# Kernel optimization log

Hardware: AMD Instinct MI355X
Metric: run time of the kernel (lower is better)

## Reference

```python
import jax, jax.numpy as jnp
import numpy as np

B, T, D, H, E, S, K = 2, 2048, 768, 1536, 8, 1, 2
STD = 0.02


def setup_inputs() -> dict:
    key = jax.random.key(0)
    ks = jax.random.split(key, 8)
    x = jax.random.normal(ks[0], (B, T, D), jnp.float32)
    router_w = jax.random.normal(ks[1], (E, D), jnp.float32) * STD
    sw1 = jax.random.normal(ks[2], (S, D, H), jnp.float32) * STD
    sw2 = jax.random.normal(ks[3], (S, D, H), jnp.float32) * STD
    sproj = jax.random.normal(ks[4], (S, H, D), jnp.float32) * STD
    ew1 = jax.random.normal(ks[5], (E, D, H), jnp.float32) * STD
    ew2 = jax.random.normal(ks[6], (E, D, H), jnp.float32) * STD
    eproj = jax.random.normal(ks[7], (E, H, D), jnp.float32) * STD
    return {"x": x, "router_w": router_w, "sw1": sw1, "sw2": sw2,
            "sproj": sproj, "ew1": ew1, "ew2": ew2, "eproj": eproj,
            "top_k": K}


def reference(x, router_w, sw1, sw2, sproj, ew1, ew2, eproj, top_k):
    n_experts = router_w.shape[0]
    # Shared experts (SwiGLU), summed over the shared-expert axis s.
    a = jnp.einsum('btd,sdh->bsth', x, sw1)
    b = jnp.einsum('btd,sdh->bsth', x, sw2)
    shared_out = jnp.einsum('bsth,shd->btd', jax.nn.silu(a) * b, sproj)  # [B,T,D]

    # Router: note the original applies softmax and calls the result `logits`,
    # returning it as the second output.
    probs = jax.nn.softmax(jnp.einsum('btd,ed->bte', x, router_w), axis=-1)  # [B,T,E]
    top_vals, top_idx = jax.lax.top_k(probs, top_k)
    weights = top_vals / jnp.sum(top_vals, axis=-1, keepdims=True)  # renormalized [B,T,K]

    # Dense combine weights: combine[b,t,e] = sum_k weights[b,t,k] * 1[top_idx[b,t,k]==e]
    combine = jnp.sum(jax.nn.one_hot(top_idx, n_experts, dtype=x.dtype)
                      * weights[..., None], axis=-2)  # [B,T,E]

    # Routed experts: compute every expert densely, then mask/weight by combine.
    ea = jnp.einsum('btd,edh->bteh', x, ew1)
    eb = jnp.einsum('btd,edh->bteh', x, ew2)
    routed = jnp.einsum('bteh,ehd,bte->btd', jax.nn.silu(ea) * eb, eproj, combine)

    return shared_out + routed, probs
```

## Files before the change

### kernel.cpp

```cpp
#include <hip/hip_runtime.h>

typedef unsigned short u16;
typedef __bf16 bf16x8 __attribute__((ext_vector_type(8)));
typedef float f32x4 __attribute__((ext_vector_type(4)));

__device__ __forceinline__ u16 f2bf(float f) {
  union { float f; unsigned u; } v; v.f = f;
  return (u16)((v.u + 0x7fffu + ((v.u >> 16) & 1u)) >> 16);
}

#define GLDS16(g, l)                                                          \
  __builtin_amdgcn_global_load_lds(                                           \
      (const __attribute__((address_space(1))) void*)(g),                     \
      (__attribute__((address_space(3))) void*)(l), 16, 0, 0)

#define SBAR()  __builtin_amdgcn_s_barrier()
#define SCHED() __builtin_amdgcn_sched_barrier(0)
#define VMCNT(n) asm volatile("s_waitcnt vmcnt(" #n ")" ::: "memory")

#define NTOK 4096
#define DIM  768
#define HID  1536
#define NEXP 8
#define CAPR 9216
#define SHB  9216
#define NSLOT 13312
#define MAXT 104


__global__ __launch_bounds__(256) void k_tr_all(const float* __restrict__ ew1,
                                                const float* __restrict__ sw1,
                                                const float* __restrict__ ew2,
                                                const float* __restrict__ sw2,
                                                const float* __restrict__ eproj,
                                                const float* __restrict__ sproj,
                                                u16* __restrict__ dstBase) {
  __shared__ u16 tile[64][65];
  constexpr size_t SL = (size_t)HID * DIM;
  const int z = blockIdx.z;
  const float* src;
  int R, C, bxx = blockIdx.x, byy = blockIdx.y;
  if (z < 9)       { src = (z < 8) ? ew1 + (size_t)z * SL : sw1; R = DIM; C = HID; }
  else if (z < 18) { const int q = z - 9;  src = (q < 8) ? ew2 + (size_t)q * SL : sw2; R = DIM; C = HID; }
  else             { const int q = z - 18; src = (q < 8) ? eproj + (size_t)q * SL : sproj;
                     R = HID; C = DIM; const int t = bxx; bxx = byy; byy = t; }
  u16* dst = dstBase + (size_t)z * SL;
  const int c0 = bxx * 64, r0 = byy * 64;
  const int tx = threadIdx.x, ty = threadIdx.y;
  #pragma unroll
  for (int i = 0; i < 16; i++)
    tile[ty + 4 * i][tx] = f2bf(src[(size_t)(r0 + ty + 4 * i) * C + c0 + tx]);
  __syncthreads();
  #pragma unroll
  for (int i = 0; i < 16; i++)
    dst[(size_t)(c0 + ty + 4 * i) * R + r0 + tx] = tile[tx][ty + 4 * i];
}

__global__ __launch_bounds__(64) void k_router(const float* __restrict__ x,
                                               const float* __restrict__ rw,
                                               float* __restrict__ probs,
                                               int* __restrict__ topIdx,
                                               float* __restrict__ topW,
                                               u16* __restrict__ xb) {
  const int t = blockIdx.x;
  const int lane = threadIdx.x;
  const float* xr = x + (size_t)t * DIM;
  u16* xbr = xb + (size_t)t * DIM;
  float acc[NEXP] = {0, 0, 0, 0, 0, 0, 0, 0};
  #pragma unroll
  for (int i = 0; i < DIM / 64; i++) {
    const int d = lane + 64 * i;
    const float xv = xr[d];
    xbr[d] = f2bf(xv);
    #pragma unroll
    for (int e = 0; e < NEXP; e++) acc[e] += xv * rw[e * DIM + d];
  }
  #pragma unroll
  for (int e = 0; e < NEXP; e++)
    #pragma unroll
    for (int s = 32; s > 0; s >>= 1) acc[e] += __shfl_xor(acc[e], s, 64);
  if (lane == 0) {
    float mx = acc[0];
    #pragma unroll
    for (int e = 1; e < NEXP; e++) mx = fmaxf(mx, acc[e]);
    float p[NEXP], sum = 0.f;
    #pragma unroll
    for (int e = 0; e < NEXP; e++) { p[e] = expf(acc[e] - mx); sum += p[e]; }
    const float inv = 1.f / sum;
    #pragma unroll
    for (int e = 0; e < NEXP; e++) p[e] *= inv;
    #pragma unroll
    for (int e = 0; e < NEXP; e++) probs[(size_t)t * NEXP + e] = p[e];
    int i1 = 0;
    #pragma unroll
    for (int e = 1; e < NEXP; e++) if (p[e] > p[i1]) i1 = e;
    int i2 = (i1 == 0) ? 1 : 0;
    #pragma unroll
    for (int e = 0; e < NEXP; e++) if (e != i1 && p[e] > p[i2]) i2 = e;
    const float s2 = 1.f / (p[i1] + p[i2]);
    topIdx[2 * t] = i1; topIdx[2 * t + 1] = i2;
    topW[2 * t] = p[i1] * s2; topW[2 * t + 1] = p[i2] * s2;
  }
}

__global__ __launch_bounds__(256) void k_build(const int* __restrict__ topIdx,
                                               const float* __restrict__ topW,
                                               int* __restrict__ listT,
                                               float* __restrict__ listW,
                                               int* __restrict__ listP,
                                               int* __restrict__ cnt) {
  const int e = blockIdx.x;
  const int tid = threadIdx.x, w = tid >> 6, lane = tid & 63;
  __shared__ int wt[4];
  int base = 0;
  for (int c = 0; c < NTOK / 256; ++c) {
    const int t = c * 256 + tid;
    const int i0 = topIdx[2 * t], i1 = topIdx[2 * t + 1];
    const int pr = (i0 == e) ? 1 : ((i1 == e) ? 2 : 0);
    const unsigned long long m = __ballot(pr != 0);
    const int wl = __popcll(m & ((1ull << lane) - 1ull));
    if (lane == 0) wt[w] = __popcll(m);
    __syncthreads();
    int wbase = 0;
    #pragma unroll
    for (int j = 0; j < 4; j++) if (j < w) wbase += wt[j];
    if (pr) {
      const int pos = base + wbase + wl;
      listT[e * NTOK + pos] = t;
      listW[e * NTOK + pos] = (pr == 1) ? topW[2 * t] : topW[2 * t + 1];
      listP[e * NTOK + pos] = pr;
    }
    base += wt[0] + wt[1] + wt[2] + wt[3];
    __syncthreads();
  }
  if (tid == 0) cnt[e] = base;
}

__global__ __launch_bounds__(256) void k_tilemap(const int* __restrict__ cnt,
                                                 const int* __restrict__ listT,
                                                 const float* __restrict__ listW,
                                                 const int* __restrict__ listP,
                                                 int* __restrict__ tileExp,
                                                 int* __restrict__ tileM0,
                                                 int* __restrict__ slotTok,
                                                 float* __restrict__ slotW,
                                                 int* __restrict__ tokSlot) {
  __shared__ int offPad[NEXP + 1];
  __shared__ int cs[NEXP];
  const int tid = threadIdx.x;
  if (tid == 0) {
    int tt = 0, acc = 0;
    for (int e = 0; e < NEXP; e++) {
      cs[e] = cnt[e];
      offPad[e] = acc;
      const int tiles = (cs[e] + 127) >> 7;
      for (int i = 0; i < tiles; i++) { tileExp[tt] = e; tileM0[tt] = acc + i * 128; tt++; }
      acc += tiles * 128;
    }
    offPad[NEXP] = acc;
    for (int i = 0; i < NTOK / 128; i++) { tileExp[tt] = NEXP; tileM0[tt] = SHB + i * 128; tt++; }
    for (; tt < MAXT; tt++) tileExp[tt] = -1;
  }
  __syncthreads();
  for (int s = tid; s < CAPR; s += 256) {
    int tok = 0; float wv = 0.f; int pp = 0;
    #pragma unroll
    for (int e = 0; e < NEXP; e++)
      if (s >= offPad[e] && s < offPad[e + 1]) {
        const int i = s - offPad[e];
        if (i < cs[e]) {
          tok = listT[e * NTOK + i];
          wv = listW[e * NTOK + i];
          pp = listP[e * NTOK + i];
        }
      }
    slotTok[s] = tok; slotW[s] = wv;
    if (pp) tokSlot[2 * tok + (pp - 1)] = s;
  }
  for (int s = tid; s < NTOK; s += 256) { slotTok[SHB + s] = s; slotW[SHB + s] = 1.f; }
}

__global__ __launch_bounds__(256, 2) void k_gemm1(const u16* __restrict__ xb,
                                                  const u16* __restrict__ w1t,
                                                  const u16* __restrict__ w2t,
                                                  const int* __restrict__ tileExp,
                                                  const int* __restrict__ tileM0,
                                                  const int* __restrict__ slotTok,
                                                  const float* __restrict__ slotW,
                                                  u16* __restrict__ hidden) {
  __shared__ alignas(16) u16 As[3][4096];
  __shared__ alignas(16) u16 B1s[3][4096];
  __shared__ alignas(16) u16 B2s[3][4096];
  const int chunk = (MAXT * (HID / 128)) >> 3;
  const int bid = blockIdx.x;
  const int wgid = (bid & 7) * chunk + (bid >> 3);
  const int bx = wgid % MAXT;
  const int by = wgid / MAXT;
  const int e = tileExp[bx];
  if (e < 0) return;
  const int m0 = tileM0[bx];
  const int nBase = by * 128;
  constexpr size_t SL = (size_t)HID * DIM;
  const u16* w1 = w1t + (size_t)e * SL;
  const u16* w2 = w2t + (size_t)e * SL;
  const int tid = threadIdx.x, w = tid >> 6, lane = tid & 63;
  const int wr = w >> 1, wc = w & 1;

  const int qrow = lane >> 2;
  const int col0 = ((lane & 3) ^ ((lane >> 3) & 3)) * 8;
  const int tok0 = slotTok[m0 + w * 32 + qrow];
  const int tok1 = slotTok[m0 + w * 32 + 16 + qrow];
  const u16* gA0 = xb + (size_t)tok0 * DIM + col0;
  const u16* gA1 = xb + (size_t)tok1 * DIM + col0;
  const u16* gB1a = w1 + (size_t)(nBase + w * 32 + qrow) * DIM + col0;
  const u16* gB1b = w1 + (size_t)(nBase + w * 32 + 16 + qrow) * DIM + col0;
  const u16* gB2a = w2 + (size_t)(nBase + w * 32 + qrow) * DIM + col0;
  const u16* gB2b = w2 + (size_t)(nBase + w * 32 + 16 + qrow) * DIM + col0;
  const int l0 = (w * 2 + 0) * 512 + lane * 8;
  const int l1 = (w * 2 + 1) * 512 + lane * 8;

  f32x4 acc1[4][4], acc2[4][4];
  const f32x4 vz = {0.f, 0.f, 0.f, 0.f};
  #pragma unroll
  for (int m = 0; m < 4; m++)
    #pragma unroll
    for (int n = 0; n < 4; n++) { acc1[m][n] = vz; acc2[m][n] = vz; }

  const int rbase = lane & 15;
  const int swz = (lane >> 4) ^ ((rbase >> 1) & 3);
  const int aoffB = (wr * 64 + rbase) * 32 + swz * 8;
  const int boffB = (wc * 64 + rbase) * 32 + swz * 8;

#define G1_STAGE(buf, kk) do {                                                \
    GLDS16(gA0  + (kk), &As[buf][l0]);  GLDS16(gA1  + (kk), &As[buf][l1]);    \
    GLDS16(gB1a + (kk), &B1s[buf][l0]); GLDS16(gB1b + (kk), &B1s[buf][l1]);   \
    GLDS16(gB2a + (kk), &B2s[buf][l0]); GLDS16(gB2b + (kk), &B2s[buf][l1]);   \
  } while (0)

#define G1_BODY(buf, vm, dostage, kk) do {                                    \
    SCHED(); VMCNT(vm); SBAR(); SCHED();                                      \
    if (dostage) { G1_STAGE((buf + 2) % 3, kk); SCHED(); }                    \
    bf16x8 av[4], b1v[4], b2v[4];                                             \
    _Pragma("unroll")                                                         \
    for (int m = 0; m < 4; m++) av[m] = *(const bf16x8*)&As[buf][aoffB + m * 512]; \
    _Pragma("unroll")                                                         \
    for (int n = 0; n < 4; n++) {                                             \
      b1v[n] = *(const bf16x8*)&B1s[buf][boffB + n * 512];                    \
      b2v[n] = *(const bf16x8*)&B2s[buf][boffB + n * 512];                    \
    }                                                                         \
    __builtin_amdgcn_s_setprio(1);                                            \
    _Pragma("unroll")                                                         \
    for (int m = 0; m < 4; m++)                                               \
      _Pragma("unroll")                                                       \
      for (int n = 0; n < 4; n++) {                                           \
        acc1[m][n] = __builtin_amdgcn_mfma_f32_16x16x32_bf16(av[m], b1v[n], acc1[m][n], 0, 0, 0); \
        acc2[m][n] = __builtin_amdgcn_mfma_f32_16x16x32_bf16(av[m], b2v[n], acc2[m][n], 0, 0, 0); \
      }                                                                       \
    __builtin_amdgcn_s_setprio(0);                                            \
  } while (0)

  G1_STAGE(0, 0);  SCHED();
  G1_STAGE(1, 32); SCHED();
  for (int t = 0; t < 21; t += 3) {
    G1_BODY(0, 6, true, (t + 2) * 32);
    G1_BODY(1, 6, true, (t + 3) * 32);
    G1_BODY(2, 6, true, (t + 4) * 32);
  }
  G1_BODY(0, 6, true, 23 * 32);
  G1_BODY(1, 6, false, 0);
  G1_BODY(2, 0, false, 0);
#undef G1_BODY
#undef G1_STAGE

  #pragma unroll
  for (int m = 0; m < 4; m++)
    #pragma unroll
    for (int r = 0; r < 4; r++) {
      const int slot = m0 + wr * 64 + m * 16 + (lane >> 4) * 4 + r;
      const float cwv = slotW[slot];
      #pragma unroll
      for (int n = 0; n < 4; n++) {
        const int hcol = nBase + wc * 64 + n * 16 + (lane & 15);
        const float v1 = acc1[m][n][r], v2 = acc2[m][n][r];
        hidden[(size_t)slot * HID + hcol] = f2bf((v1 / (1.f + __expf(-v1))) * v2 * cwv);
      }
    }
}

__global__ __launch_bounds__(256, 3) void k_gemm2(const u16* __restrict__ hid,
                                                  const u16* __restrict__ pjt,
                                                  const int* __restrict__ tileExp,
                                                  const int* __restrict__ tileM0,
                                                  float* __restrict__ g2) {
  __shared__ alignas(16) u16 As[3][4096];
  __shared__ alignas(16) u16 Bs[3][4096];
  const int chunk = (MAXT * (DIM / 128)) >> 3;
  const int bid = blockIdx.x;
  const int wgid = (bid & 7) * chunk + (bid >> 3);
  const int bx = wgid % MAXT;
  const int by = wgid / MAXT;
  const int e = tileExp[bx];
  if (e < 0) return;
  const int m0 = tileM0[bx];
  const int nBase = by * 128;
  constexpr size_t SL = (size_t)HID * DIM;
  const u16* pj = pjt + (size_t)e * SL;
  const int tid = threadIdx.x, w = tid >> 6, lane = tid & 63;
  const int wr = w >> 1, wc = w & 1;

  const int qrow = lane >> 2;
  const int col0 = ((lane & 3) ^ ((lane >> 3) & 3)) * 8;
  const u16* gA0 = hid + (size_t)(m0 + w * 32 + qrow) * HID + col0;
  const u16* gA1 = hid + (size_t)(m0 + w * 32 + 16 + qrow) * HID + col0;
  const u16* gBa = pj + (size_t)(nBase + w * 32 + qrow) * HID + col0;
  const u16* gBb = pj + (size_t)(nBase + w * 32 + 16 + qrow) * HID + col0;
  const int l0 = (w * 2 + 0) * 512 + lane * 8;
  const int l1 = (w * 2 + 1) * 512 + lane * 8;

  f32x4 acc[4][4];
  const f32x4 vz = {0.f, 0.f, 0.f, 0.f};
  #pragma unroll
  for (int m = 0; m < 4; m++)
    #pragma unroll
    for (int n = 0; n < 4; n++) acc[m][n] = vz;

  const int rbase = lane & 15;
  const int swz = (lane >> 4) ^ ((rbase >> 1) & 3);
  const int aoffB = (wr * 64 + rbase) * 32 + swz * 8;
  const int boffB = (wc * 64 + rbase) * 32 + swz * 8;

#define G2_STAGE(buf, kk) do {                                                \
    GLDS16(gA0 + (kk), &As[buf][l0]); GLDS16(gA1 + (kk), &As[buf][l1]);       \
    GLDS16(gBa + (kk), &Bs[buf][l0]); GLDS16(gBb + (kk), &Bs[buf][l1]);       \
  } while (0)

#define G2_BODY(buf, vm, dostage, kk) do {                                    \
    SCHED(); VMCNT(vm); SBAR(); SCHED();                                      \
    if (dostage) { G2_STAGE((buf + 2) % 3, kk); SCHED(); }                    \
    bf16x8 av[4], bv[4];                                                      \
    _Pragma("unroll")                                                         \
    for (int m = 0; m < 4; m++) av[m] = *(const bf16x8*)&As[buf][aoffB + m * 512]; \
    _Pragma("unroll")                                                         \
    for (int n = 0; n < 4; n++) bv[n] = *(const bf16x8*)&Bs[buf][boffB + n * 512]; \
    __builtin_amdgcn_s_setprio(1);                                            \
    _Pragma("unroll")                                                         \
    for (int m = 0; m < 4; m++)                                               \
      _Pragma("unroll")                                                       \
      for (int n = 0; n < 4; n++)                                             \
        acc[m][n] = __builtin_amdgcn_mfma_f32_16x16x32_bf16(av[m], bv[n], acc[m][n], 0, 0, 0); \
    __builtin_amdgcn_s_setprio(0);                                            \
  } while (0)

  G2_STAGE(0, 0);  SCHED();
  G2_STAGE(1, 32); SCHED();
  for (int t = 0; t < 45; t += 3) {
    G2_BODY(0, 4, true, (t + 2) * 32);
    G2_BODY(1, 4, true, (t + 3) * 32);
    G2_BODY(2, 4, true, (t + 4) * 32);
  }
  G2_BODY(0, 4, true, 47 * 32);
  G2_BODY(1, 4, false, 0);
  G2_BODY(2, 0, false, 0);
#undef G2_BODY
#undef G2_STAGE

  #pragma unroll
  for (int m = 0; m < 4; m++)
    #pragma unroll
    for (int r = 0; r < 4; r++) {
      const int slot = m0 + wr * 64 + m * 16 + (lane >> 4) * 4 + r;
      #pragma unroll
      for (int n = 0; n < 4; n++) {
        const int dcol = nBase + wc * 64 + n * 16 + (lane & 15);
        g2[(size_t)slot * DIM + dcol] = acc[m][n][r];
      }
    }
}

__global__ __launch_bounds__(192) void k_combine(const float* __restrict__ g2,
                                                 const int* __restrict__ tokSlot,
                                                 float* __restrict__ out) {
  const int t = blockIdx.x, d4 = threadIdx.x;
  const int sA = tokSlot[2 * t], sB = tokSlot[2 * t + 1];
  const int lo = sA < sB ? sA : sB;
  const int hi = sA < sB ? sB : sA;
  const float4 a = ((const float4*)(g2 + (size_t)lo * DIM))[d4];
  const float4 b = ((const float4*)(g2 + (size_t)hi * DIM))[d4];
  const float4 c = ((const float4*)(g2 + (size_t)(SHB + t) * DIM))[d4];
  float4 o;
  o.x = a.x + b.x + c.x; o.y = a.y + b.y + c.y;
  o.z = a.z + b.z + c.z; o.w = a.w + b.w + c.w;
  ((float4*)(out + (size_t)t * DIM))[d4] = o;
}

extern "C" void kernel_launch(void* const* d_in, const int* in_sizes, int n_in,
                              void* d_out, int out_size, void* d_ws, size_t ws_size,
                              hipStream_t stream) {
  const float* x     = (const float*)d_in[0];
  const float* rw    = (const float*)d_in[1];
  const float* sw1   = (const float*)d_in[2];
  const float* sw2   = (const float*)d_in[3];
  const float* sproj = (const float*)d_in[4];
  const float* ew1   = (const float*)d_in[5];
  const float* ew2   = (const float*)d_in[6];
  const float* eproj = (const float*)d_in[7];
  float* out   = (float*)d_out;
  float* probs = out + (size_t)NTOK * DIM;

  constexpr size_t SL = (size_t)HID * DIM;
  constexpr size_t off_xb   = 0;
  constexpr size_t off_w1t  = 6291456;
  constexpr size_t off_w2t  = off_w1t + 2 * 9 * SL;
  constexpr size_t off_pjt  = off_w2t + 2 * 9 * SL;
  constexpr size_t off_hid  = off_pjt + 2 * 9 * SL;
  constexpr size_t off_g2   = off_hid + (size_t)NSLOT * HID * 2;
  constexpr size_t off_meta = off_g2 + (size_t)NSLOT * DIM * 4;

  char* ws = (char*)d_ws;
  u16*   xb   = (u16*)(ws + off_xb);
  u16*   w1t  = (u16*)(ws + off_w1t);
  u16*   w2t  = (u16*)(ws + off_w2t);
  u16*   pjt  = (u16*)(ws + off_pjt);
  u16*   hid  = (u16*)(ws + off_hid);
  float* g2   = (float*)(ws + off_g2);
  char*  meta = ws + off_meta;
  int*   topIdx  = (int*)meta;
  float* topW    = (float*)(meta + 32768);
  int*   listT   = (int*)(meta + 65536);
  float* listW   = (float*)(meta + 196608);
  int*   listP   = (int*)(meta + 327680);
  int*   cnt     = (int*)(meta + 458752);
  int*   tileExp = (int*)(meta + 459264);
  int*   tileM0  = (int*)(meta + 459776);
  int*   slotTok = (int*)(meta + 460288);
  float* slotW   = (float*)(meta + 513536);
  int*   tokSlot = (int*)(meta + 566784);

  k_router<<<NTOK, 64, 0, stream>>>(x, rw, probs, topIdx, topW, xb);
  k_tr_all<<<dim3(HID / 64, DIM / 64, 27), dim3(64, 4), 0, stream>>>(
      ew1, sw1, ew2, sw2, eproj, sproj, w1t);

  k_build<<<NEXP, 256, 0, stream>>>(topIdx, topW, listT, listW, listP, cnt);
  k_tilemap<<<1, 256, 0, stream>>>(cnt, listT, listW, listP, tileExp, tileM0,
                                   slotTok, slotW, tokSlot);

  k_gemm1<<<MAXT * (HID / 128), 256, 0, stream>>>(xb, w1t, w2t, tileExp, tileM0,
                                                  slotTok, slotW, hid);
  k_gemm2<<<MAXT * (DIM / 128), 256, 0, stream>>>(hid, pjt, tileExp, tileM0, g2);
  k_combine<<<NTOK, 192, 0, stream>>>(g2, tokSlot, out);
}
```

Measured before the change: 224.0 us.

## Use 256-row expert tiles with 512-thread gemm1 and two-stage split-K pipeline

The first grouped GEMM moves from 128-row tiles with 256 threads to 256-row tiles with 512 threads (8 waves). Each block loads one weight tile and reuses it across twice as many gathered token rows. The mainloop becomes a hand-scheduled double-buffered pipeline that splits each K step into halves and interleaves MFMA with async global-to-LDS loads. Expert capacity is padded to 256 rows, so more padding work is done, and the second GEMM gets a derived 128-row tile map. The larger LDS footprint (128KB per block) and higher register pressure may limit occupancy.

Result: faster. 215.3 us (-3.9%).

```diff
diff --git a/kernel.cpp b/kernel.cpp
--- a/kernel.cpp
+++ b/kernel.cpp
@@ -22,11 +22,11 @@
 #define DIM  768
 #define HID  1536
 #define NEXP 8
-#define CAPR 9216
-#define SHB  9216
-#define NSLOT 13312
-#define MAXT 104
-
+#define CAPR 10240
+#define SHB  10240
+#define NSLOT 14336
+#define MAXT1 56
+#define MAXT2 112
 
 __global__ __launch_bounds__(256) void k_tr_all(const float* __restrict__ ew1,
                                                 const float* __restrict__ sw1,
@@ -140,8 +140,8 @@
                                                  const int* __restrict__ listT,
                                                  const float* __restrict__ listW,
                                                  const int* __restrict__ listP,
-                                                 int* __restrict__ tileExp,
-                                                 int* __restrict__ tileM0,
+                                                 int* __restrict__ tE1, int* __restrict__ tM1,
+                                                 int* __restrict__ tE2, int* __restrict__ tM2,
                                                  int* __restrict__ slotTok,
                                                  float* __restrict__ slotW,
                                                  int* __restrict__ tokSlot) {
@@ -153,13 +153,17 @@
     for (int e = 0; e < NEXP; e++) {
       cs[e] = cnt[e];
       offPad[e] = acc;
-      const int tiles = (cs[e] + 127) >> 7;
-      for (int i = 0; i < tiles; i++) { tileExp[tt] = e; tileM0[tt] = acc + i * 128; tt++; }
-      acc += tiles * 128;
+      const int tiles = (cs[e] + 255) >> 8;
+      for (int i = 0; i < tiles; i++) { tE1[tt] = e; tM1[tt] = acc + i * 256; tt++; }
+      acc += tiles * 256;
     }
     offPad[NEXP] = acc;
-    for (int i = 0; i < NTOK / 128; i++) { tileExp[tt] = NEXP; tileM0[tt] = SHB + i * 128; tt++; }
-    for (; tt < MAXT; tt++) tileExp[tt] = -1;
+    for (int i = 0; i < NTOK / 256; i++) { tE1[tt] = NEXP; tM1[tt] = SHB + i * 256; tt++; }
+    for (; tt < MAXT1; tt++) { tE1[tt] = -1; tM1[tt] = 0; }
+    for (int j = 0; j < MAXT1; j++) {
+      tE2[2 * j] = tE1[j];     tM2[2 * j] = tM1[j];
+      tE2[2 * j + 1] = tE1[j]; tM2[2 * j + 1] = tM1[j] + 128;
+    }
   }
   __syncthreads();
   for (int s = tid; s < CAPR; s += 256) {
@@ -180,25 +184,21 @@
   for (int s = tid; s < NTOK; s += 256) { slotTok[SHB + s] = s; slotW[SHB + s] = 1.f; }
 }
 
-__global__ __launch_bounds__(256, 2) void k_gemm1(const u16* __restrict__ xb,
+__global__ __launch_bounds__(512, 2) void k_gemm1(const u16* __restrict__ xb,
                                                   const u16* __restrict__ w1t,
                                                   const u16* __restrict__ w2t,
-                                                  const int* __restrict__ tileExp,
-                                                  const int* __restrict__ tileM0,
+                                                  const int* __restrict__ tE1,
+                                                  const int* __restrict__ tM1,
                                                   const int* __restrict__ slotTok,
                                                   const float* __restrict__ slotW,
                                                   u16* __restrict__ hidden) {
-  __shared__ alignas(16) u16 As[3][4096];
-  __shared__ alignas(16) u16 B1s[3][4096];
-  __shared__ alignas(16) u16 B2s[3][4096];
-  const int chunk = (MAXT * (HID / 128)) >> 3;
+  __shared__ alignas(16) u16 L[2][32768];
   const int bid = blockIdx.x;
-  const int wgid = (bid & 7) * chunk + (bid >> 3);
-  const int bx = wgid % MAXT;
-  const int by = wgid / MAXT;
-  const int e = tileExp[bx];
+  const int wgid = (bid & 7) * 84 + (bid >> 3);
+  const int bx = wgid % MAXT1, by = wgid / MAXT1;
+  const int e = tE1[bx];
   if (e < 0) return;
-  const int m0 = tileM0[bx];
+  const int m0 = tM1[bx];
   const int nBase = by * 128;
   constexpr size_t SL = (size_t)HID * DIM;
   const u16* w1 = w1t + (size_t)e * SL;
@@ -206,18 +206,20 @@
   const int tid = threadIdx.x, w = tid >> 6, lane = tid & 63;
   const int wr = w >> 1, wc = w & 1;
 
-  const int qrow = lane >> 2;
-  const int col0 = ((lane & 3) ^ ((lane >> 3) & 3)) * 8;
-  const int tok0 = slotTok[m0 + w * 32 + qrow];
-  const int tok1 = slotTok[m0 + w * 32 + 16 + qrow];
-  const u16* gA0 = xb + (size_t)tok0 * DIM + col0;
-  const u16* gA1 = xb + (size_t)tok1 * DIM + col0;
-  const u16* gB1a = w1 + (size_t)(nBase + w * 32 + qrow) * DIM + col0;
-  const u16* gB1b = w1 + (size_t)(nBase + w * 32 + 16 + qrow) * DIM + col0;
-  const u16* gB2a = w2 + (size_t)(nBase + w * 32 + qrow) * DIM + col0;
-  const u16* gB2b = w2 + (size_t)(nBase + w * 32 + 16 + qrow) * DIM + col0;
-  const int l0 = (w * 2 + 0) * 512 + lane * 8;
-  const int l1 = (w * 2 + 1) * 512 + lane * 8;
+  const int srow = tid >> 2;
+  const int kcol = ((tid & 3) ^ ((tid >> 3) & 3)) * 8;
+  const int tokA0 = slotTok[m0 + srow];
+  const int tokA1 = slotTok[m0 + 128 + srow];
+  const u16* gA0 = xb + (size_t)tokA0 * DIM + kcol;
+  const u16* gA1 = xb + (size_t)tokA1 * DIM + kcol;
+  const u16* gB1 = w1 + (size_t)(nBase + srow) * DIM + kcol;
+  const u16* gB2 = w2 + (size_t)(nBase + srow) * DIM + kcol;
+  const int dA0 = tid * 8, dA1 = 4096 + tid * 8, dB = tid * 8;
+
+  const int rl = lane & 15;
+  const int kq = lane >> 4;
+  const int aBase = (wr * 64 + rl) * 32 + (kq ^ ((rl >> 1) & 3)) * 8;
+  const int bBase = (wc * 64 + rl) * 32 + (kq ^ ((rl >> 1) & 3)) * 8;
 
   f32x4 acc1[4][4], acc2[4][4];
   const f32x4 vz = {0.f, 0.f, 0.f, 0.f};
@@ -226,51 +228,66 @@
     #pragma unroll
     for (int n = 0; n < 4; n++) { acc1[m][n] = vz; acc2[m][n] = vz; }
 
-  const int rbase = lane & 15;
-  const int swz = (lane >> 4) ^ ((rbase >> 1) & 3);
-  const int aoffB = (wr * 64 + rbase) * 32 + swz * 8;
-  const int boffB = (wc * 64 + rbase) * 32 + swz * 8;
-
-#define G1_STAGE(buf, kk) do {                                                \
-    GLDS16(gA0  + (kk), &As[buf][l0]);  GLDS16(gA1  + (kk), &As[buf][l1]);    \
-    GLDS16(gB1a + (kk), &B1s[buf][l0]); GLDS16(gB1b + (kk), &B1s[buf][l1]);   \
-    GLDS16(gB2a + (kk), &B2s[buf][l0]); GLDS16(gB2b + (kk), &B2s[buf][l1]);   \
-  } while (0)
-
-#define G1_BODY(buf, vm, dostage, kk) do {                                    \
-    SCHED(); VMCNT(vm); SBAR(); SCHED();                                      \
-    if (dostage) { G1_STAGE((buf + 2) % 3, kk); SCHED(); }                    \
-    bf16x8 av[4], b1v[4], b2v[4];                                             \
-    _Pragma("unroll")                                                         \
-    for (int m = 0; m < 4; m++) av[m] = *(const bf16x8*)&As[buf][aoffB + m * 512]; \
-    _Pragma("unroll")                                                         \
+#define G1_STA(d, koff, kh) do {                                              \
+    GLDS16(gA0 + (koff), &L[d][(kh) * 8192 + dA0]);                           \
+    GLDS16(gA1 + (koff), &L[d][(kh) * 8192 + dA1]); } while (0)
+#define G1_STB(d, koff, kh) do {                                              \
+    GLDS16(gB1 + (koff), &L[d][16384 + (kh) * 4096 + dB]);                    \
+    GLDS16(gB2 + (koff), &L[d][24576 + (kh) * 4096 + dB]); } while (0)
+#define G1_RDB(d, kh) do { _Pragma("unroll")                                  \
     for (int n = 0; n < 4; n++) {                                             \
-      b1v[n] = *(const bf16x8*)&B1s[buf][boffB + n * 512];                    \
-      b2v[n] = *(const bf16x8*)&B2s[buf][boffB + n * 512];                    \
-    }                                                                         \
-    __builtin_amdgcn_s_setprio(1);                                            \
-    _Pragma("unroll")                                                         \
-    for (int m = 0; m < 4; m++)                                               \
-      _Pragma("unroll")                                                       \
-      for (int n = 0; n < 4; n++) {                                           \
-        acc1[m][n] = __builtin_amdgcn_mfma_f32_16x16x32_bf16(av[m], b1v[n], acc1[m][n], 0, 0, 0); \
-        acc2[m][n] = __builtin_amdgcn_mfma_f32_16x16x32_bf16(av[m], b2v[n], acc2[m][n], 0, 0, 0); \
-      }                                                                       \
-    __builtin_amdgcn_s_setprio(0);                                            \
-  } while (0)
-
-  G1_STAGE(0, 0);  SCHED();
-  G1_STAGE(1, 32); SCHED();
-  for (int t = 0; t < 21; t += 3) {
-    G1_BODY(0, 6, true, (t + 2) * 32);
-    G1_BODY(1, 6, true, (t + 3) * 32);
-    G1_BODY(2, 6, true, (t + 4) * 32);
-  }
-  G1_BODY(0, 6, true, 23 * 32);
-  G1_BODY(1, 6, false, 0);
-  G1_BODY(2, 0, false, 0);
-#undef G1_BODY
-#undef G1_STAGE
+      b1v[n] = *(const bf16x8*)&L[d][16384 + (kh) * 4096 + bBase + n * 512];  \
+      b2v[n] = *(const bf16x8*)&L[d][24576 + (kh) * 4096 + bBase + n * 512]; } } while (0)
+#define G1_RDA(d, kh, mp) do { _Pragma("unroll")                              \
+    for (int j = 0; j < 2; j++)                                               \
+      av[j] = *(const bf16x8*)&L[d][(kh) * 8192 + aBase + ((mp) * 2 + j) * 512]; } while (0)
+#define G1_MM(mp) do { __builtin_amdgcn_s_setprio(1);                         \
+    _Pragma("unroll") for (int j = 0; j < 2; j++)                             \
+      _Pragma("unroll") for (int n = 0; n < 4; n++) {                         \
+        acc1[(mp) * 2 + j][n] = __builtin_amdgcn_mfma_f32_16x16x32_bf16(av[j], b1v[n], acc1[(mp) * 2 + j][n], 0, 0, 0); \
+        acc2[(mp) * 2 + j][n] = __builtin_amdgcn_mfma_f32_16x16x32_bf16(av[j], b2v[n], acc2[(mp) * 2 + j][n], 0, 0, 0); } \
+    __builtin_amdgcn_s_setprio(0); } while (0)
+
+  G1_STA(0, 0, 0);  G1_STB(0, 0, 0);
+  G1_STA(0, 32, 1); G1_STB(0, 32, 1);
+  G1_STA(1, 64, 0); G1_STB(1, 64, 0);
+  SCHED(); VMCNT(8); SBAR(); SCHED();
+
+  bf16x8 av[2], b1v[4], b2v[4];
+  for (int i = 0; i < 5; i++) {
+    const int kOff = i * 128;
+    G1_RDB(0, 0); G1_RDA(0, 0, 0); SCHED(); G1_STA(1, kOff + 96, 1); SCHED();
+    G1_MM(0); SCHED(); SBAR(); SCHED();
+    G1_RDA(0, 0, 1); SCHED(); G1_STB(1, kOff + 96, 1); SCHED();
+    G1_MM(1); SCHED(); VMCNT(8); SBAR(); SCHED();
+    G1_RDB(0, 1); G1_RDA(0, 1, 0); SCHED(); G1_STA(0, kOff + 128, 0); SCHED();
+    G1_MM(0); SCHED(); SBAR(); SCHED();
+    G1_RDA(0, 1, 1); SCHED(); G1_STB(0, kOff + 128, 0); SCHED();
+    G1_MM(1); SCHED(); VMCNT(8); SBAR(); SCHED();
+    G1_RDB(1, 0); G1_RDA(1, 0, 0); SCHED(); G1_STA(0, kOff + 160, 1); SCHED();
+    G1_MM(0); SCHED(); SBAR(); SCHED();
+    G1_RDA(1, 0, 1); SCHED(); G1_STB(0, kOff + 160, 1); SCHED();
+    G1_MM(1); SCHED(); VMCNT(8); SBAR(); SCHED();
+    G1_RDB(1, 1); G1_RDA(1, 1, 0); SCHED(); G1_STA(1, kOff + 192, 0); SCHED();
+    G1_MM(0); SCHED(); SBAR(); SCHED();
+    G1_RDA(1, 1, 1); SCHED(); G1_STB(1, kOff + 192, 0); SCHED();
+    G1_MM(1); SCHED(); VMCNT(8); SBAR(); SCHED();
+  }
+  G1_RDB(0, 0); G1_RDA(0, 0, 0); SCHED(); G1_STA(1, 736, 1); SCHED();
+  G1_MM(0); SCHED(); SBAR(); SCHED();
+  G1_RDA(0, 0, 1); SCHED(); G1_STB(1, 736, 1); SCHED();
+  G1_MM(1); SCHED(); VMCNT(8); SBAR(); SCHED();
+  G1_RDB(0, 1); G1_RDA(0, 1, 0); SCHED(); G1_MM(0); SCHED(); SBAR(); SCHED();
+  G1_RDA(0, 1, 1); SCHED(); G1_MM(1); SCHED(); VMCNT(4); SBAR(); SCHED();
+  G1_RDB(1, 0); G1_RDA(1, 0, 0); SCHED(); G1_MM(0); SCHED(); SBAR(); SCHED();
+  G1_RDA(1, 0, 1); SCHED(); G1_MM(1); SCHED(); VMCNT(0); SBAR(); SCHED();
+  G1_RDB(1, 1); G1_RDA(1, 1, 0); SCHED(); G1_MM(0); SCHED(); SBAR(); SCHED();
+  G1_RDA(1, 1, 1); SCHED(); G1_MM(1);
+#undef G1_STA
+#undef G1_STB
+#undef G1_RDB
+#undef G1_RDA
+#undef G1_MM
 
   #pragma unroll
   for (int m = 0; m < 4; m++)
@@ -289,19 +306,18 @@
 
 __global__ __launch_bounds__(256, 3) void k_gemm2(const u16* __restrict__ hid,
                                                   const u16* __restrict__ pjt,
-                                                  const int* __restrict__ tileExp,
-                                                  const int* __restrict__ tileM0,
+                                                  const int* __restrict__ tE2,
+                                                  const int* __restrict__ tM2,
                                                   float* __restrict__ g2) {
   __shared__ alignas(16) u16 As[3][4096];
   __shared__ alignas(16) u16 Bs[3][4096];
-  const int chunk = (MAXT * (DIM / 128)) >> 3;
   const int bid = blockIdx.x;
-  const int wgid = (bid & 7) * chunk + (bid >> 3);
-  const int bx = wgid % MAXT;
-  const int by = wgid / MAXT;
-  const int e = tileExp[bx];
+  const int wgid = (bid & 7) * 84 + (bid >> 3);
+  const int bx = wgid % MAXT2;
+  const int by = wgid / MAXT2;
+  const int e = tE2[bx];
   if (e < 0) return;
-  const int m0 = tileM0[bx];
+  const int m0 = tM2[bx];
   const int nBase = by * 128;
   constexpr size_t SL = (size_t)HID * DIM;
   const u16* pj = pjt + (size_t)e * SL;
@@ -314,8 +330,7 @@
   const u16* gA1 = hid + (size_t)(m0 + w * 32 + 16 + qrow) * HID + col0;
   const u16* gBa = pj + (size_t)(nBase + w * 32 + qrow) * HID + col0;
   const u16* gBb = pj + (size_t)(nBase + w * 32 + 16 + qrow) * HID + col0;
-  const int l0 = (w * 2 + 0) * 512 + lane * 8;
-  const int l1 = (w * 2 + 1) * 512 + lane * 8;
+  const int l0 = (w * 128 + lane) * 8, l1 = (w * 128 + lane + 64) * 8;
 
   f32x4 acc[4][4];
   const f32x4 vz = {0.f, 0.f, 0.f, 0.f};
@@ -430,22 +445,24 @@
   float* listW   = (float*)(meta + 196608);
   int*   listP   = (int*)(meta + 327680);
   int*   cnt     = (int*)(meta + 458752);
-  int*   tileExp = (int*)(meta + 459264);
-  int*   tileM0  = (int*)(meta + 459776);
-  int*   slotTok = (int*)(meta + 460288);
-  float* slotW   = (float*)(meta + 513536);
-  int*   tokSlot = (int*)(meta + 566784);
+  int*   tE1     = (int*)(meta + 459264);
+  int*   tM1     = (int*)(meta + 459776);
+  int*   tE2     = (int*)(meta + 460288);
+  int*   tM2     = (int*)(meta + 460800);
+  int*   slotTok = (int*)(meta + 461312);
+  float* slotW   = (float*)(meta + 518656);
+  int*   tokSlot = (int*)(meta + 576000);
 
   k_router<<<NTOK, 64, 0, stream>>>(x, rw, probs, topIdx, topW, xb);
   k_tr_all<<<dim3(HID / 64, DIM / 64, 27), dim3(64, 4), 0, stream>>>(
       ew1, sw1, ew2, sw2, eproj, sproj, w1t);
 
   k_build<<<NEXP, 256, 0, stream>>>(topIdx, topW, listT, listW, listP, cnt);
-  k_tilemap<<<1, 256, 0, stream>>>(cnt, listT, listW, listP, tileExp, tileM0,
+  k_tilemap<<<1, 256, 0, stream>>>(cnt, listT, listW, listP, tE1, tM1, tE2, tM2,
                                    slotTok, slotW, tokSlot);
 
-  k_gemm1<<<MAXT * (HID / 128), 256, 0, stream>>>(xb, w1t, w2t, tileExp, tileM0,
-                                                  slotTok, slotW, hid);
-  k_gemm2<<<MAXT * (DIM / 128), 256, 0, stream>>>(hid, pjt, tileExp, tileM0, g2);
+  k_gemm1<<<MAXT1 * (HID / 128), 512, 0, stream>>>(xb, w1t, w2t, tE1, tM1,
+                                                   slotTok, slotW, hid);
+  k_gemm2<<<MAXT2 * (DIM / 128), 256, 0, stream>>>(hid, pjt, tE2, tM2, g2);
   k_combine<<<NTOK, 192, 0, stream>>>(g2, tokSlot, out);
 }
```
